# Performance work log

Measured on AMD Instinct MI355X. Metric: run time of the kernel, lower is better.

## Reference

```python
import jax, jax.numpy as jnp
import numpy as np

B, N, H, W, P = 32, 6, 512, 512, 512
SCALE, ASPECT, MIN_PH = 0.5, 1.0, 60.0


def setup_inputs() -> dict:
    key = jax.random.key(0)
    k1, k2, k3, k4, k5, k6 = jax.random.split(key, 6)
    images = jax.random.normal(k1, (B, H, W, 3), jnp.float32)
    patch = jax.random.normal(k2, (P, P, 3), jnp.float32)
    # person bboxes (ymin, xmin, ymax, xmax) in pixels, fully inside the image
    hsz = jax.random.uniform(k3, (B, N), jnp.float32, 120.0, 400.0)
    wsz = jax.random.uniform(k4, (B, N), jnp.float32, 120.0, 400.0)
    ymin = jax.random.uniform(k5, (B, N), jnp.float32) * (H - hsz)
    xmin = jax.random.uniform(k6, (B, N), jnp.float32) * (W - wsz)
    boxes = jnp.stack([ymin, xmin, ymin + hsz, xmin + wsz], axis=-1)
    return {"images": images, "boxes": boxes, "patch": patch}


def _patch_boxes(boxes):
    # Patcher.create: derive (ymin_patch, xmin_patch, patch_h, patch_w) from each bbox
    ymin, xmin, ymax, xmax = (boxes[..., 0], boxes[..., 1], boxes[..., 2], boxes[..., 3])
    h = ymax - ymin
    w = xmax - xmin
    pw = h * SCALE
    ph = ASPECT * pw
    oy = ymin + h * 0.5
    ox = xmin + w * 0.5
    yp = jnp.maximum(oy - ph * 0.5, 0.0)
    xp = jnp.maximum(ox - pw * 0.5, 0.0)
    yp = jnp.where(yp + ph > H, H - ph, yp)
    xp = jnp.where(xp + pw > W, W - pw, xp)
    valid = ph > MIN_PH  # ragged filter -> mask
    return jnp.stack([yp, xp, ph, pw], axis=-1), valid


def _paste_one(img, patch, box, valid):
    # fused gather(resize bilinear, half-pixel centers) + scatter of the patch into img
    Pn = patch.shape[0]
    b = box.astype(jnp.int32)  # tf.cast truncation
    y0b, x0b, h, w = b[0], b[1], b[2], b[3]
    hf = jnp.maximum(h, 1).astype(jnp.float32)
    wf = jnp.maximum(w, 1).astype(jnp.float32)
    dy = jnp.arange(img.shape[0]) - y0b
    dx = jnp.arange(img.shape[1]) - x0b
    sy = jnp.clip((dy.astype(jnp.float32) + 0.5) * (Pn / hf) - 0.5, 0.0, Pn - 1.0)
    sx = jnp.clip((dx.astype(jnp.float32) + 0.5) * (Pn / wf) - 0.5, 0.0, Pn - 1.0)
    yl = jnp.floor(sy).astype(jnp.int32); yh = jnp.minimum(yl + 1, Pn - 1); wy = sy - yl
    xl = jnp.floor(sx).astype(jnp.int32); xh = jnp.minimum(xl + 1, Pn - 1); wx = sx - xl
    # separable bilinear: rows [H, P, 3] then cols -> [H, W, 3]
    rows = patch[yl] * (1.0 - wy)[:, None, None] + patch[yh] * wy[:, None, None]
    val = rows[:, xl] * (1.0 - wx)[None, :, None] + rows[:, xh] * wx[None, :, None]
    inside = ((dy >= 0) & (dy < h))[:, None] & ((dx >= 0) & (dx < w))[None, :] & valid
    return jnp.where(inside[..., None], val, img)


def reference(images, boxes, patch):
    pboxes, valid = _patch_boxes(boxes)
    def step(imgs, xs):
        bx, v = xs  # [B,4], [B]
        imgs = jax.vmap(lambda im, b_, v_: _paste_one(im, patch, b_, v_))(imgs, bx, v)
        return imgs, None
    # sequential over patches (later patches overwrite earlier, as in the tf while_loop)
    out, _ = jax.lax.scan(step, images, (jnp.transpose(pboxes, (1, 0, 2)), valid.T))
    return out
```

## Files before the change

kernel.cpp:

```cpp
#include <hip/hip_runtime.h>


#define Bn 32
#define Nn 6
#define Hh 512
#define Ww 512
#define Pp 512

typedef float f32x4u __attribute__((ext_vector_type(4), aligned(4)));
typedef float f32x2u __attribute__((ext_vector_type(2), aligned(4)));

struct BoxP {
    int   y0b, x0b, hI, wI;
    float syscale, winv;
    int   valid, pad;
};

__global__ __launch_bounds__(192) void box_setup_kernel(
    const float* __restrict__ boxes,
    BoxP* __restrict__ bp)
{
    const int i = threadIdx.x;
    if (i >= Bn * Nn) return;
    const float ymin = boxes[i * 4 + 0];
    const float xmin = boxes[i * 4 + 1];
    const float ymax = boxes[i * 4 + 2];
    const float xmax = boxes[i * 4 + 3];
    const float h  = ymax - ymin;
    const float w  = xmax - xmin;
    const float pw = h * 0.5f;
    const float ph = 1.0f * pw;
    const float oy = ymin + h * 0.5f;
    const float ox = xmin + w * 0.5f;
    float yp = fmaxf(oy - ph * 0.5f, 0.0f);
    float xp = fmaxf(ox - pw * 0.5f, 0.0f);
    yp = (yp + ph > (float)Hh) ? ((float)Hh - ph) : yp;
    xp = (xp + pw > (float)Ww) ? ((float)Ww - pw) : xp;

    BoxP p;
    p.y0b = (int)yp;
    p.x0b = (int)xp;
    p.hI  = (int)ph;
    p.wI  = (int)pw;
    const float hf = (float)(p.hI > 1 ? p.hI : 1);
    const float wf = (float)(p.wI > 1 ? p.wI : 1);
    p.syscale = (float)Pp / hf;
    p.winv    = (float)Pp / wf;
    p.valid   = (ph > 60.0f) ? 1 : 0;
    p.pad     = 0;
    bp[i] = p;
}

__global__ __launch_bounds__(256) void patch_attack_kernel(
    const float* __restrict__ images,
    const BoxP* __restrict__ bparams,
    const float* __restrict__ patch,
    float* __restrict__ out)
{
    const int tid = threadIdx.x;
    const int gid = blockIdx.x * 256 + tid;
    const int b   = __builtin_amdgcn_readfirstlane(gid >> 17);
    const int rem = gid & 131071;
    const int y   = __builtin_amdgcn_readfirstlane(rem >> 8);
    const int x0  = (rem & 255) << 1;

    const BoxP* __restrict__ bp = bparams + b * Nn;

    int   bid0 = -1, bid1 = -1;
    int   off0 = 0,  off1 = 0;
    float wx0 = 0.f, wy0 = 0.f, wx1 = 0.f, wy1 = 0.f;

    #pragma unroll
    for (int n = Nn - 1; n >= 0; --n) {
        const int y0b = bp[n].y0b;
        const int hI  = bp[n].hI;
        const int dy  = y - y0b;
        if (!(bp[n].valid && dy >= 0 && dy < hI)) continue;

        const int   x0b     = bp[n].x0b;
        const int   wI      = bp[n].wI;
        const float syscale = bp[n].syscale;
        const float winv    = bp[n].winv;

        float sy = ((float)dy + 0.5f) * syscale - 0.5f;
        sy = fminf(fmaxf(sy, 0.0f), (float)(Pp - 1));
        int yl = (int)sy;
        yl = (yl > Pp - 2) ? (Pp - 2) : yl;
        const float wyv = sy - (float)yl;
        const int rl = yl * (Pp * 3 * 4);

        {
            const int dx = x0 - x0b;
            float sx = ((float)dx + 0.5f) * winv - 0.5f;
            sx = fminf(fmaxf(sx, 0.0f), (float)(Pp - 1));
            int xl = (int)sx;
            xl = (xl > Pp - 2) ? (Pp - 2) : xl;
            const float wxv = sx - (float)xl;
            if ((dx >= 0) & (dx < wI) & (bid0 < 0)) {
                bid0 = n; off0 = rl + xl * 12; wx0 = wxv; wy0 = wyv;
            }
        }
        {
            const int dx = x0 + 1 - x0b;
            float sx = ((float)dx + 0.5f) * winv - 0.5f;
            sx = fminf(fmaxf(sx, 0.0f), (float)(Pp - 1));
            int xl = (int)sx;
            xl = (xl > Pp - 2) ? (Pp - 2) : xl;
            const float wxv = sx - (float)xl;
            if ((dx >= 0) & (dx < wI) & (bid1 < 0)) {
                bid1 = n; off1 = rl + xl * 12; wx1 = wxv; wy1 = wyv;
            }
        }
    }

    const bool c0 = bid0 >= 0, c1 = bid1 >= 0;
    f32x4u i0 = {0.f, 0.f, 0.f, 0.f};
    f32x2u i1 = {0.f, 0.f};
    const size_t fbase = (size_t)gid * 6;
    if (!(c0 & c1)) {
        i0 = *(const f32x4u*)(images + fbase);
        i1 = *(const f32x2u*)(images + fbase + 4);
    }

    float pr[6] = {0.f, 0.f, 0.f, 0.f, 0.f, 0.f};
    const char* __restrict__ pb = (const char*)patch;
    if (__any(c0 | c1)) {
        const f32x4u a00 = *(const f32x4u*)(pb + off0);
        const f32x2u a01 = *(const f32x2u*)(pb + off0 + 16);
        const f32x4u b00 = *(const f32x4u*)(pb + off0 + 6144);
        const f32x2u b01 = *(const f32x2u*)(pb + off0 + 6160);
        const f32x4u a10 = *(const f32x4u*)(pb + off1);
        const f32x2u a11 = *(const f32x2u*)(pb + off1 + 16);
        const f32x4u b10 = *(const f32x4u*)(pb + off1 + 6144);
        const f32x2u b11 = *(const f32x2u*)(pb + off1 + 6160);
        {
            const float omy = 1.0f - wy0, omx = 1.0f - wx0;
            const float A[6]  = {a00.x, a00.y, a00.z, a00.w, a01.x, a01.y};
            const float Bv[6] = {b00.x, b00.y, b00.z, b00.w, b01.x, b01.y};
            #pragma unroll
            for (int c = 0; c < 3; ++c)
                pr[c] = (A[c]     * omy + Bv[c]     * wy0) * omx
                      + (A[3 + c] * omy + Bv[3 + c] * wy0) * wx0;
        }
        {
            const float omy = 1.0f - wy1, omx = 1.0f - wx1;
            const float A[6]  = {a10.x, a10.y, a10.z, a10.w, a11.x, a11.y};
            const float Bv[6] = {b10.x, b10.y, b10.z, b10.w, b11.x, b11.y};
            #pragma unroll
            for (int c = 0; c < 3; ++c)
                pr[3 + c] = (A[c]     * omy + Bv[c]     * wy1) * omx
                          + (A[3 + c] * omy + Bv[3 + c] * wy1) * wx1;
        }
    }

    float r[6];
    r[0] = c0 ? pr[0] : i0.x;
    r[1] = c0 ? pr[1] : i0.y;
    r[2] = c0 ? pr[2] : i0.z;
    r[3] = c1 ? pr[3] : i0.w;
    r[4] = c1 ? pr[4] : i1.x;
    r[5] = c1 ? pr[5] : i1.y;

    f32x4u v0; v0.x = r[0]; v0.y = r[1]; v0.z = r[2]; v0.w = r[3];
    f32x2u v1; v1.x = r[4]; v1.y = r[5];
    *(f32x4u*)(out + fbase)     = v0;
    *(f32x2u*)(out + fbase + 4) = v1;
}

extern "C" void kernel_launch(void* const* d_in, const int* in_sizes, int n_in,
                              void* d_out, int out_size, void* d_ws, size_t ws_size,
                              hipStream_t stream) {
    const float* images = (const float*)d_in[0];
    const float* boxes  = (const float*)d_in[1];
    const float* patch  = (const float*)d_in[2];
    float* out = (float*)d_out;
    BoxP* bp = (BoxP*)d_ws;

    box_setup_kernel<<<1, 192, 0, stream>>>(boxes, bp);

    patch_attack_kernel<<<16384, 256, 0, stream>>>(images, bp, patch, out);
}
```

Measured before the change: 194.9 us.

## Stage patch source rows in LDS per block row, nontemporal image loads

Each block now handles one full image row and, for each box covering that row, cooperatively loads the two needed patch source rows (yl and yl+1, 12 KB) into shared memory. The bilinear taps are then read from LDS instead of issuing scattered unaligned global loads per thread. Image loads become nontemporal. This adds block-wide syncs per covering box (up to six per row) and serializes loading and compute within a block.

```diff
diff --git a/kernel.cpp b/kernel.cpp
--- a/kernel.cpp
+++ b/kernel.cpp
@@ -7,6 +7,7 @@
 #define Ww 512
 #define Pp 512
 
+typedef float f32x4 __attribute__((ext_vector_type(4)));
 typedef float f32x4u __attribute__((ext_vector_type(4), aligned(4)));
 typedef float f32x2u __attribute__((ext_vector_type(2), aligned(4)));
 
@@ -57,17 +58,18 @@
     const float* __restrict__ patch,
     float* __restrict__ out)
 {
+    __shared__ f32x4 lds4[768];
+    float* __restrict__ ldsf = (float*)lds4;
+
     const int tid = threadIdx.x;
-    const int gid = blockIdx.x * 256 + tid;
-    const int b   = __builtin_amdgcn_readfirstlane(gid >> 17);
-    const int rem = gid & 131071;
-    const int y   = __builtin_amdgcn_readfirstlane(rem >> 8);
-    const int x0  = (rem & 255) << 1;
+    const int b   = blockIdx.x >> 9;
+    const int y   = blockIdx.x & 511;
+    const int x0  = tid << 1;
 
     const BoxP* __restrict__ bp = bparams + b * Nn;
 
     int   bid0 = -1, bid1 = -1;
-    int   off0 = 0,  off1 = 0;
+    int   xls0 = 0,  xls1 = 0;
     float wx0 = 0.f, wy0 = 0.f, wx1 = 0.f, wy1 = 0.f;
 
     #pragma unroll
@@ -87,7 +89,6 @@
         int yl = (int)sy;
         yl = (yl > Pp - 2) ? (Pp - 2) : yl;
         const float wyv = sy - (float)yl;
-        const int rl = yl * (Pp * 3 * 4);
 
         {
             const int dx = x0 - x0b;
@@ -97,7 +98,7 @@
             xl = (xl > Pp - 2) ? (Pp - 2) : xl;
             const float wxv = sx - (float)xl;
             if ((dx >= 0) & (dx < wI) & (bid0 < 0)) {
-                bid0 = n; off0 = rl + xl * 12; wx0 = wxv; wy0 = wyv;
+                bid0 = n; xls0 = xl; wx0 = wxv; wy0 = wyv;
             }
         }
         {
@@ -108,7 +109,7 @@
             xl = (xl > Pp - 2) ? (Pp - 2) : xl;
             const float wxv = sx - (float)xl;
             if ((dx >= 0) & (dx < wI) & (bid1 < 0)) {
-                bid1 = n; off1 = rl + xl * 12; wx1 = wxv; wy1 = wyv;
+                bid1 = n; xls1 = xl; wx1 = wxv; wy1 = wyv;
             }
         }
     }
@@ -116,40 +117,52 @@
     const bool c0 = bid0 >= 0, c1 = bid1 >= 0;
     f32x4u i0 = {0.f, 0.f, 0.f, 0.f};
     f32x2u i1 = {0.f, 0.f};
-    const size_t fbase = (size_t)gid * 6;
+    const size_t fbase = ((size_t)blockIdx.x * 512 + (size_t)x0) * 3;
     if (!(c0 & c1)) {
-        i0 = *(const f32x4u*)(images + fbase);
-        i1 = *(const f32x2u*)(images + fbase + 4);
+        i0 = __builtin_nontemporal_load((const f32x4u*)(images + fbase));
+        i1 = __builtin_nontemporal_load((const f32x2u*)(images + fbase + 4));
     }
 
     float pr[6] = {0.f, 0.f, 0.f, 0.f, 0.f, 0.f};
-    const char* __restrict__ pb = (const char*)patch;
-    if (__any(c0 | c1)) {
-        const f32x4u a00 = *(const f32x4u*)(pb + off0);
-        const f32x2u a01 = *(const f32x2u*)(pb + off0 + 16);
-        const f32x4u b00 = *(const f32x4u*)(pb + off0 + 6144);
-        const f32x2u b01 = *(const f32x2u*)(pb + off0 + 6160);
-        const f32x4u a10 = *(const f32x4u*)(pb + off1);
-        const f32x2u a11 = *(const f32x2u*)(pb + off1 + 16);
-        const f32x4u b10 = *(const f32x4u*)(pb + off1 + 6144);
-        const f32x2u b11 = *(const f32x2u*)(pb + off1 + 6160);
-        {
+    #pragma unroll
+    for (int n = Nn - 1; n >= 0; --n) {
+        const int y0b = bp[n].y0b;
+        const int hI  = bp[n].hI;
+        const int dy  = y - y0b;
+        if (!(bp[n].valid && dy >= 0 && dy < hI)) continue;
+
+        const int hit0 = (bid0 == n), hit1 = (bid1 == n);
+        if (!__syncthreads_or(hit0 | hit1)) continue;
+
+        float sy = ((float)dy + 0.5f) * bp[n].syscale - 0.5f;
+        sy = fminf(fmaxf(sy, 0.0f), (float)(Pp - 1));
+        int yl = (int)sy;
+        yl = (yl > Pp - 2) ? (Pp - 2) : yl;
+
+        const char* __restrict__ src = (const char*)patch + (size_t)yl * 6144;
+        const f32x4 t0 = *(const f32x4*)(src + (size_t)tid * 16);
+        const f32x4 t1 = *(const f32x4*)(src + 4096 + (size_t)tid * 16);
+        const f32x4 t2 = *(const f32x4*)(src + 8192 + (size_t)tid * 16);
+        lds4[tid]       = t0;
+        lds4[tid + 256] = t1;
+        lds4[tid + 512] = t2;
+        __syncthreads();
+
+        if (hit0) {
+            const int o = xls0 * 3;
             const float omy = 1.0f - wy0, omx = 1.0f - wx0;
-            const float A[6]  = {a00.x, a00.y, a00.z, a00.w, a01.x, a01.y};
-            const float Bv[6] = {b00.x, b00.y, b00.z, b00.w, b01.x, b01.y};
             #pragma unroll
             for (int c = 0; c < 3; ++c)
-                pr[c] = (A[c]     * omy + Bv[c]     * wy0) * omx
-                      + (A[3 + c] * omy + Bv[3 + c] * wy0) * wx0;
+                pr[c] = (ldsf[o + c]     * omy + ldsf[1536 + o + c]     * wy0) * omx
+                      + (ldsf[o + 3 + c] * omy + ldsf[1536 + o + 3 + c] * wy0) * wx0;
         }
-        {
+        if (hit1) {
+            const int o = xls1 * 3;
             const float omy = 1.0f - wy1, omx = 1.0f - wx1;
-            const float A[6]  = {a10.x, a10.y, a10.z, a10.w, a11.x, a11.y};
-            const float Bv[6] = {b10.x, b10.y, b10.z, b10.w, b11.x, b11.y};
             #pragma unroll
             for (int c = 0; c < 3; ++c)
-                pr[3 + c] = (A[c]     * omy + Bv[c]     * wy1) * omx
-                          + (A[3 + c] * omy + Bv[3 + c] * wy1) * wx1;
+                pr[3 + c] = (ldsf[o + c]     * omy + ldsf[1536 + o + c]     * wy1) * omx
+                          + (ldsf[o + 3 + c] * omy + ldsf[1536 + o + 3 + c] * wy1) * wx1;
         }
     }
 
```

Result: faster. 188.4 us (-3.3%).
